# Kernel optimization log

Hardware: AMD Instinct MI355X
Metric: run time of the kernel (lower is better)

The kernel has to match this reference:

```python
import jax, jax.numpy as jnp
import numpy as np
from jax import lax


def setup_inputs() -> dict:
    key = jax.random.key(0)
    k1, k2 = jax.random.split(key)
    B, C, H, W = 4, 128, 128, 256
    features_1 = jax.random.normal(k1, (B, C, H, W), dtype=jnp.float32)
    features_2 = jax.random.normal(k2, (B, C, H, W), dtype=jnp.float32)
    return {"features_1": features_1, "features_2": features_2, "lvls": 64}


def reference(features_1, features_2, lvls):
    # Cost volume: cost[b, i, h, w] = mean_c f1[b,c,h,w] * f2[b,c,h,w-i] for w >= i, else 0.
    B, C, H, W = features_1.shape
    # Left-pad f2 along width with (lvls-1) zeros so shifted slices are static-size.
    f2_pad = jnp.pad(features_2, ((0, 0), (0, 0), (0, 0), (lvls - 1, 0)))

    def body(carry, i):
        # slice starting at (lvls-1-i) gives f2 shifted right by disparity i, zeros where w < i
        f2_shift = lax.dynamic_slice_in_dim(f2_pad, lvls - 1 - i, W, axis=3)
        cost_i = jnp.mean(features_1 * f2_shift, axis=1)  # [B, H, W]
        return carry, cost_i

    _, cost = lax.scan(body, None, jnp.arange(lvls))  # [lvls, B, H, W]
    return jnp.moveaxis(cost, 0, 1)  # [B, lvls, H, W]
```

## Files before the change

### kernel.cpp

```cpp
#include <hip/hip_runtime.h>
#include <hip/hip_bf16.h>


#define BDIM 4
#define CDIM 128
#define HDIM 128
#define WDIM 256
#define LVLS 64
#define HW   (HDIM * WDIM)
#define CHW  (CDIM * HDIM * WDIM)

typedef short  bf16x8 __attribute__((ext_vector_type(8)));
typedef float  f32x16 __attribute__((ext_vector_type(16)));

__device__ __forceinline__ short f2bf(float f) {
    __hip_bfloat16 h = __float2bfloat16(f);
    return __builtin_bit_cast(short, h);
}

__global__ __launch_bounds__(512, 4) void cost_volume_kernel(
    const float* __restrict__ f1, const float* __restrict__ f2,
    float* __restrict__ out)
{
    __shared__ float cost_lds[LVLS * WDIM];

    const int tid  = threadIdx.x;
    const int lane = tid & 63;
    const int wv   = tid >> 6;
    const int wg   = blockIdx.x;
    const int b    = wg >> 7;
    const int h    = wg & (HDIM - 1);

    const float* __restrict__ f1bh = f1 + (size_t)b * CHW + (size_t)h * WDIM;
    const float* __restrict__ f2bh = f2 + (size_t)b * CHW + (size_t)h * WDIM;

    const int wl    = lane & 31;
    const int wglob = wv * 32 + wl;
    const int koff  = (lane >> 5) * 8;

    const int tp0c = (wv - 2 < 0) ? 0 : wv - 2;
    const int tp1c = (wv - 1 < 0) ? 0 : wv - 1;
    const int tp2c = wv;

    const float* pB  = f1bh + (size_t)koff * HW + wglob;
    const float* pA0 = f2bh + (size_t)koff * HW + tp0c * 32 + wl;
    const float* pA1 = f2bh + (size_t)koff * HW + tp1c * 32 + wl;
    const float* pA2 = f2bh + (size_t)koff * HW + tp2c * 32 + wl;

    f32x16 acc0 = (f32x16)0.0f, acc1 = (f32x16)0.0f, acc2 = (f32x16)0.0f;

    #pragma unroll
    for (int kk = 0; kk < 8; ++kk) {
        const size_t kb = (size_t)(kk * 16) * HW;

        float rb[8], ra0[8], ra1[8], ra2[8];
        #pragma unroll
        for (int j = 0; j < 8; ++j) rb[j]  = pB [kb + (size_t)j * HW];
        #pragma unroll
        for (int j = 0; j < 8; ++j) ra0[j] = pA0[kb + (size_t)j * HW];
        #pragma unroll
        for (int j = 0; j < 8; ++j) ra1[j] = pA1[kb + (size_t)j * HW];
        #pragma unroll
        for (int j = 0; j < 8; ++j) ra2[j] = pA2[kb + (size_t)j * HW];

        bf16x8 fb, fa0, fa1, fa2;
        #pragma unroll
        for (int j = 0; j < 8; ++j) {
            fb[j]  = f2bf(rb[j]);
            fa0[j] = f2bf(ra0[j]);
            fa1[j] = f2bf(ra1[j]);
            fa2[j] = f2bf(ra2[j]);
        }

        acc0 = __builtin_amdgcn_mfma_f32_32x32x16_bf16(fa0, fb, acc0, 0, 0, 0);
        acc1 = __builtin_amdgcn_mfma_f32_32x32x16_bf16(fa1, fb, acc1, 0, 0, 0);
        acc2 = __builtin_amdgcn_mfma_f32_32x32x16_bf16(fa2, fb, acc2, 0, 0, 0);
    }


    if (wv < 2 && lane < 32) {
        #pragma unroll 1
        for (int i = 1; i < LVLS; ++i)
            if (i > wglob) cost_lds[i * WDIM + wglob] = 0.0f;
    }

    const int rbase = 4 * (lane >> 5);
    {
        const f32x16* accs[3] = { &acc0, &acc1, &acc2 };
        #pragma unroll
        for (int t = 0; t < 3; ++t) {
            const int tp = wv - 2 + t;
            if (tp >= 0) {
                const f32x16 a = *accs[t];
                #pragma unroll
                for (int r = 0; r < 16; ++r) {
                    const int prow = tp * 32 + (r & 3) + 8 * (r >> 2) + rbase;
                    const int i = wglob - prow;
                    if (i >= 0 && i < LVLS)
                        cost_lds[i * WDIM + wglob] = a[r] * (1.0f / CDIM);
                }
            }
        }
    }

    __syncthreads();

    const size_t obase = ((size_t)b * LVLS) * HW + (size_t)h * WDIM;
    #pragma unroll
    for (int rep = 0; rep < 8; ++rep) {
        const int idx = rep * 512 + tid;
        const int row = idx >> 6;
        const int w4  = idx & 63;
        const float4 v = *reinterpret_cast<const float4*>(&cost_lds[row * WDIM + w4 * 4]);
        *reinterpret_cast<float4*>(out + obase + (size_t)row * HW + w4 * 4) = v;
    }
}

extern "C" void kernel_launch(void* const* d_in, const int* in_sizes, int n_in,
                              void* d_out, int out_size, void* d_ws, size_t ws_size,
                              hipStream_t stream) {
    const float* f1 = (const float*)d_in[0];
    const float* f2 = (const float*)d_in[1];
    float* out = (float*)d_out;
    cost_volume_kernel<<<dim3(BDIM * HDIM), dim3(512), 0, stream>>>(f1, f2, out);
}
```

Measured before the change: 31.94 us.

## Stage feature tiles into LDS via async global_load_lds with double buffering

Each 16-channel slice of f1 and f2 is now loaded cooperatively into double-buffered LDS using global_load_lds. The next slice is prefetched while MFMAs run on the current one. This replaces direct per-lane global loads, which fetched each f2 column up to three times, so every byte is read from global memory once and load latency overlaps compute. In exchange there is a __syncthreads per iteration, extra LDS reads with possible bank conflicts, and reuse of the same LDS buffer for the cost output.

```diff
diff --git a/kernel.cpp b/kernel.cpp
--- a/kernel.cpp
+++ b/kernel.cpp
@@ -13,6 +13,9 @@
 typedef short  bf16x8 __attribute__((ext_vector_type(8)));
 typedef float  f32x16 __attribute__((ext_vector_type(16)));
 
+typedef __attribute__((address_space(1))) const unsigned int guint;
+typedef __attribute__((address_space(3))) unsigned int luint;
+
 __device__ __forceinline__ short f2bf(float f) {
     __hip_bfloat16 h = __float2bfloat16(f);
     return __builtin_bit_cast(short, h);
@@ -22,7 +25,7 @@
     const float* __restrict__ f1, const float* __restrict__ f2,
     float* __restrict__ out)
 {
-    __shared__ float cost_lds[LVLS * WDIM];
+    __shared__ float lds[16384];
 
     const int tid  = threadIdx.x;
     const int lane = tid & 63;
@@ -40,43 +43,57 @@
 
     const int tp0c = (wv - 2 < 0) ? 0 : wv - 2;
     const int tp1c = (wv - 1 < 0) ? 0 : wv - 1;
-    const int tp2c = wv;
-
-    const float* pB  = f1bh + (size_t)koff * HW + wglob;
-    const float* pA0 = f2bh + (size_t)koff * HW + tp0c * 32 + wl;
-    const float* pA1 = f2bh + (size_t)koff * HW + tp1c * 32 + wl;
-    const float* pA2 = f2bh + (size_t)koff * HW + tp2c * 32 + wl;
+    const int c0 = tp0c * 32 + wl;
+    const int c1 = tp1c * 32 + wl;
+    const int c2 = wv * 32 + wl;
 
     f32x16 acc0 = (f32x16)0.0f, acc1 = (f32x16)0.0f, acc2 = (f32x16)0.0f;
 
+    const int r0 = wv * 2;
+    #define STAGE(bb, kk)                                                        \
+        do {                                                                     \
+            _Pragma("unroll")                                                    \
+            for (int rr = 0; rr < 2; ++rr) {                                     \
+                const int r = r0 + rr;                                           \
+                const float* g1 = f1bh + (size_t)((kk) * 16 + r) * HW + lane * 4;\
+                const float* g2 = f2bh + (size_t)((kk) * 16 + r) * HW + lane * 4;\
+                float* l1 = &lds[(bb) * 8192 + r * 256];                         \
+                float* l2 = &lds[(bb) * 8192 + 4096 + r * 256];                  \
+                __builtin_amdgcn_global_load_lds((guint*)g1, (luint*)l1, 16, 0, 0);\
+                __builtin_amdgcn_global_load_lds((guint*)g2, (luint*)l2, 16, 0, 0);\
+            }                                                                    \
+        } while (0)
+
+    STAGE(0, 0);
+    __syncthreads();
+
     #pragma unroll
     for (int kk = 0; kk < 8; ++kk) {
-        const size_t kb = (size_t)(kk * 16) * HW;
+        const int bb = kk & 1;
+        if (kk < 7) STAGE(bb ^ 1, kk + 1);
 
-        float rb[8], ra0[8], ra1[8], ra2[8];
-        #pragma unroll
-        for (int j = 0; j < 8; ++j) rb[j]  = pB [kb + (size_t)j * HW];
-        #pragma unroll
-        for (int j = 0; j < 8; ++j) ra0[j] = pA0[kb + (size_t)j * HW];
-        #pragma unroll
-        for (int j = 0; j < 8; ++j) ra1[j] = pA1[kb + (size_t)j * HW];
-        #pragma unroll
-        for (int j = 0; j < 8; ++j) ra2[j] = pA2[kb + (size_t)j * HW];
+        const float* L1 = &lds[bb * 8192];
+        const float* L2 = &lds[bb * 8192 + 4096];
 
         bf16x8 fb, fa0, fa1, fa2;
         #pragma unroll
         for (int j = 0; j < 8; ++j) {
-            fb[j]  = f2bf(rb[j]);
-            fa0[j] = f2bf(ra0[j]);
-            fa1[j] = f2bf(ra1[j]);
-            fa2[j] = f2bf(ra2[j]);
+            const int k = koff + j;
+            fb[j]  = f2bf(L1[k * 256 + wglob]);
+            fa0[j] = f2bf(L2[k * 256 + c0]);
+            fa1[j] = f2bf(L2[k * 256 + c1]);
+            fa2[j] = f2bf(L2[k * 256 + c2]);
         }
 
         acc0 = __builtin_amdgcn_mfma_f32_32x32x16_bf16(fa0, fb, acc0, 0, 0, 0);
         acc1 = __builtin_amdgcn_mfma_f32_32x32x16_bf16(fa1, fb, acc1, 0, 0, 0);
         acc2 = __builtin_amdgcn_mfma_f32_32x32x16_bf16(fa2, fb, acc2, 0, 0, 0);
+
+        __syncthreads();
     }
 
+
+    float* cost_lds = lds;
 
     if (wv < 2 && lane < 32) {
         #pragma unroll 1
```

Measured after the change: 32.40 us. No clear change (+1.4%).

## Stage bf16-packed channel slices through double-buffered LDS with prefetched vector loads

Applied to the files above, without the earlier changes.

Replaces per-lane scalar global loads, where each f2 element was loaded up to three times by different waves, with cooperative float4 global loads. Each wave loads two channel rows, packs them to bf16 pairs and writes them into a double-buffered LDS stage; MFMA operands are then read from LDS. Loads are issued up to three stages ahead, with barriers between stages. Output stores become nontemporal. This adds per-stage block barriers and LDS traffic in exchange for coalesced, deduplicated global reads.

```diff
diff --git a/kernel.cpp b/kernel.cpp
--- a/kernel.cpp
+++ b/kernel.cpp
@@ -10,19 +10,24 @@
 #define HW   (HDIM * WDIM)
 #define CHW  (CDIM * HDIM * WDIM)
 
-typedef short  bf16x8 __attribute__((ext_vector_type(8)));
-typedef float  f32x16 __attribute__((ext_vector_type(16)));
+typedef short    bf16x8 __attribute__((ext_vector_type(8)));
+typedef float    f32x16 __attribute__((ext_vector_type(16)));
+typedef float    f32x4  __attribute__((ext_vector_type(4)));
+typedef unsigned u32x4  __attribute__((ext_vector_type(4)));
 
-__device__ __forceinline__ short f2bf(float f) {
-    __hip_bfloat16 h = __float2bfloat16(f);
-    return __builtin_bit_cast(short, h);
+__device__ __forceinline__ unsigned packbf(float lo, float hi) {
+    unsigned a = (unsigned)(unsigned short)__builtin_bit_cast(unsigned short, __float2bfloat16(lo));
+    unsigned b = (unsigned)(unsigned short)__builtin_bit_cast(unsigned short, __float2bfloat16(hi));
+    return a | (b << 16);
 }
 
 __global__ __launch_bounds__(512, 4) void cost_volume_kernel(
     const float* __restrict__ f1, const float* __restrict__ f2,
     float* __restrict__ out)
 {
-    __shared__ float cost_lds[LVLS * WDIM];
+    __shared__ __align__(16) char lds_raw[65536];
+    unsigned* stage = (unsigned*)lds_raw;
+    float*    cost  = (float*)lds_raw;
 
     const int tid  = threadIdx.x;
     const int lane = tid & 63;
@@ -36,52 +41,84 @@
 
     const int wl    = lane & 31;
     const int wglob = wv * 32 + wl;
-    const int koff  = (lane >> 5) * 8;
+    const int krow  = (lane >> 5) * 4;
 
-    const int tp0c = (wv - 2 < 0) ? 0 : wv - 2;
-    const int tp1c = (wv - 1 < 0) ? 0 : wv - 1;
-    const int tp2c = wv;
-
-    const float* pB  = f1bh + (size_t)koff * HW + wglob;
-    const float* pA0 = f2bh + (size_t)koff * HW + tp0c * 32 + wl;
-    const float* pA1 = f2bh + (size_t)koff * HW + tp1c * 32 + wl;
-    const float* pA2 = f2bh + (size_t)koff * HW + tp2c * 32 + wl;
+    const int c0 = ((wv - 2 < 0) ? 0 : wv - 2) * 32 + wl;
+    const int c1 = ((wv - 1 < 0) ? 0 : wv - 1) * 32 + wl;
+    const int c2 = wv * 32 + wl;
 
     f32x16 acc0 = (f32x16)0.0f, acc1 = (f32x16)0.0f, acc2 = (f32x16)0.0f;
 
+    f32x4 L1a[2], L1b[2], L2a[2], L2b[2];
+
+    #define ISSUE(s) do {                                                          \
+        const float* g1 = f1bh + (size_t)((s) * 16 + 2 * wv) * HW + lane * 4;      \
+        const float* g2 = f2bh + (size_t)((s) * 16 + 2 * wv) * HW + lane * 4;      \
+        L1a[(s) & 1] = *(const f32x4*)g1; L1b[(s) & 1] = *(const f32x4*)(g1 + HW); \
+        L2a[(s) & 1] = *(const f32x4*)g2; L2b[(s) & 1] = *(const f32x4*)(g2 + HW); \
+    } while (0)
+
+    #define WRITE(s) do {                                                          \
+        const int bb_ = (s) & 1;                                                   \
+        unsigned* p1 = stage + bb_ * 4096 + wv * 256 + (lane << 2);                \
+        u32x4 w1 = { packbf(L1a[bb_].x, L1b[bb_].x), packbf(L1a[bb_].y, L1b[bb_].y),\
+                     packbf(L1a[bb_].z, L1b[bb_].z), packbf(L1a[bb_].w, L1b[bb_].w) };\
+        *(u32x4*)p1 = w1;                                                          \
+        u32x4 w2 = { packbf(L2a[bb_].x, L2b[bb_].x), packbf(L2a[bb_].y, L2b[bb_].y),\
+                     packbf(L2a[bb_].z, L2b[bb_].z), packbf(L2a[bb_].w, L2b[bb_].w) };\
+        *(u32x4*)(p1 + 2048) = w2;                                                 \
+    } while (0)
+
+    ISSUE(0); ISSUE(1);
+    WRITE(0);
+    ISSUE(2);
+    asm volatile("s_waitcnt lgkmcnt(0)" ::: "memory");
+    __builtin_amdgcn_sched_barrier(0);
+    __builtin_amdgcn_s_barrier();
+    __builtin_amdgcn_sched_barrier(0);
+
     #pragma unroll
     for (int kk = 0; kk < 8; ++kk) {
-        const size_t kb = (size_t)(kk * 16) * HW;
+        if (kk < 7) WRITE(kk + 1);
+        if (kk + 3 <= 7) ISSUE(kk + 3);
 
-        float rb[8], ra0[8], ra1[8], ra2[8];
+        const int bb = kk & 1;
+        const unsigned* sb = stage + bb * 4096;
+        u32x4 wb, wa0, wa1, wa2;
         #pragma unroll
-        for (int j = 0; j < 8; ++j) rb[j]  = pB [kb + (size_t)j * HW];
-        #pragma unroll
-        for (int j = 0; j < 8; ++j) ra0[j] = pA0[kb + (size_t)j * HW];
-        #pragma unroll
-        for (int j = 0; j < 8; ++j) ra1[j] = pA1[kb + (size_t)j * HW];
-        #pragma unroll
-        for (int j = 0; j < 8; ++j) ra2[j] = pA2[kb + (size_t)j * HW];
+        for (int d = 0; d < 4; ++d) {
+            wb[d]  = sb[(krow + d) * 256 + wglob];
+            wa0[d] = sb[2048 + (krow + d) * 256 + c0];
+            wa1[d] = sb[2048 + (krow + d) * 256 + c1];
+            wa2[d] = sb[2048 + (krow + d) * 256 + c2];
+        }
+        asm volatile("s_waitcnt lgkmcnt(0)" ::: "memory");
+        __builtin_amdgcn_sched_barrier(0);
 
-        bf16x8 fb, fa0, fa1, fa2;
-        #pragma unroll
-        for (int j = 0; j < 8; ++j) {
-            fb[j]  = f2bf(rb[j]);
-            fa0[j] = f2bf(ra0[j]);
-            fa1[j] = f2bf(ra1[j]);
-            fa2[j] = f2bf(ra2[j]);
-        }
-
+        const bf16x8 fb  = __builtin_bit_cast(bf16x8, wb);
+        const bf16x8 fa0 = __builtin_bit_cast(bf16x8, wa0);
+        const bf16x8 fa1 = __builtin_bit_cast(bf16x8, wa1);
+        const bf16x8 fa2 = __builtin_bit_cast(bf16x8, wa2);
         acc0 = __builtin_amdgcn_mfma_f32_32x32x16_bf16(fa0, fb, acc0, 0, 0, 0);
         acc1 = __builtin_amdgcn_mfma_f32_32x32x16_bf16(fa1, fb, acc1, 0, 0, 0);
         acc2 = __builtin_amdgcn_mfma_f32_32x32x16_bf16(fa2, fb, acc2, 0, 0, 0);
+
+        if (kk < 7) {
+            __builtin_amdgcn_sched_barrier(0);
+            __builtin_amdgcn_s_barrier();
+            __builtin_amdgcn_sched_barrier(0);
+        }
     }
 
+    #undef ISSUE
+    #undef WRITE
+
+    __syncthreads();
 
     if (wv < 2 && lane < 32) {
         #pragma unroll 1
         for (int i = 1; i < LVLS; ++i)
-            if (i > wglob) cost_lds[i * WDIM + wglob] = 0.0f;
+            if (i > wglob) cost[i * WDIM + wglob] = 0.0f;
     }
 
     const int rbase = 4 * (lane >> 5);
@@ -97,7 +134,7 @@
                     const int prow = tp * 32 + (r & 3) + 8 * (r >> 2) + rbase;
                     const int i = wglob - prow;
                     if (i >= 0 && i < LVLS)
-                        cost_lds[i * WDIM + wglob] = a[r] * (1.0f / CDIM);
+                        cost[i * WDIM + wglob] = a[r] * (1.0f / CDIM);
                 }
             }
         }
@@ -111,8 +148,8 @@
         const int idx = rep * 512 + tid;
         const int row = idx >> 6;
         const int w4  = idx & 63;
-        const float4 v = *reinterpret_cast<const float4*>(&cost_lds[row * WDIM + w4 * 4]);
-        *reinterpret_cast<float4*>(out + obase + (size_t)row * HW + w4 * 4) = v;
+        const f32x4 v = *reinterpret_cast<const f32x4*>(&cost[row * WDIM + w4 * 4]);
+        __builtin_nontemporal_store(v, reinterpret_cast<f32x4*>(out + obase + (size_t)row * HW + w4 * 4));
     }
 }
 
```

Result: no change. 31.46 us (-1.5%).

## Split each row into single-wave blocks with per-strip LDS and nontemporal stores

Applied to the files above, without the earlier changes.

Each 512-thread workgroup per (b,h) row becomes eight independent 64-thread blocks, one per 32-column strip. Each block keeps a 64x32 LDS strip, so the workgroup barrier becomes a wave-local LDS fence. Block indices are remapped so that consecutive blocks land on different rows. Output writes now use nontemporal stores. The aim is to remove barrier stalls and the large per-block LDS footprint, and to improve occupancy and scheduling. In exchange there are eight times as many tiny blocks with more launch granularity, and the f2 data shared between neighbouring strips is no longer reused within a block.

```diff
diff --git a/kernel.cpp b/kernel.cpp
--- a/kernel.cpp
+++ b/kernel.cpp
@@ -9,45 +9,54 @@
 #define LVLS 64
 #define HW   (HDIM * WDIM)
 #define CHW  (CDIM * HDIM * WDIM)
+#define NWORK (BDIM * HDIM * 8)
 
-typedef short  bf16x8 __attribute__((ext_vector_type(8)));
-typedef float  f32x16 __attribute__((ext_vector_type(16)));
+typedef short    bf16x8 __attribute__((ext_vector_type(8)));
+typedef float    f32x16 __attribute__((ext_vector_type(16)));
+typedef float    f32x4  __attribute__((ext_vector_type(4)));
 
 __device__ __forceinline__ short f2bf(float f) {
     __hip_bfloat16 h = __float2bfloat16(f);
     return __builtin_bit_cast(short, h);
 }
 
-__global__ __launch_bounds__(512, 4) void cost_volume_kernel(
+__device__ __forceinline__ void lds_fence() {
+    asm volatile("s_waitcnt lgkmcnt(0)" ::: "memory");
+    __builtin_amdgcn_sched_barrier(0);
+}
+
+__global__ __launch_bounds__(64, 4) void cost_volume_kernel(
     const float* __restrict__ f1, const float* __restrict__ f2,
     float* __restrict__ out)
 {
-    __shared__ float cost_lds[LVLS * WDIM];
+    __shared__ float strip[LVLS * 32];
 
-    const int tid  = threadIdx.x;
-    const int lane = tid & 63;
-    const int wv   = tid >> 6;
-    const int wg   = blockIdx.x;
-    const int b    = wg >> 7;
-    const int h    = wg & (HDIM - 1);
+    const int lane = threadIdx.x;
+
+    const int bid  = blockIdx.x;
+    const int work = (bid & 7) * (NWORK / 8) + (bid >> 3);
+
+    const int wt = work & 7;
+    const int h  = (work >> 3) & (HDIM - 1);
+    const int b  = work >> 10;
 
     const float* __restrict__ f1bh = f1 + (size_t)b * CHW + (size_t)h * WDIM;
     const float* __restrict__ f2bh = f2 + (size_t)b * CHW + (size_t)h * WDIM;
 
     const int wl    = lane & 31;
-    const int wglob = wv * 32 + wl;
+    const int wglob = wt * 32 + wl;
     const int koff  = (lane >> 5) * 8;
 
-    const int tp0c = (wv - 2 < 0) ? 0 : wv - 2;
-    const int tp1c = (wv - 1 < 0) ? 0 : wv - 1;
-    const int tp2c = wv;
+    const int c0 = ((wt - 2 < 0) ? 0 : wt - 2) * 32 + wl;
+    const int c1 = ((wt - 1 < 0) ? 0 : wt - 1) * 32 + wl;
+    const int c2 = wt * 32 + wl;
+
+    f32x16 acc0 = (f32x16)0.0f, acc1 = (f32x16)0.0f, acc2 = (f32x16)0.0f;
 
     const float* pB  = f1bh + (size_t)koff * HW + wglob;
-    const float* pA0 = f2bh + (size_t)koff * HW + tp0c * 32 + wl;
-    const float* pA1 = f2bh + (size_t)koff * HW + tp1c * 32 + wl;
-    const float* pA2 = f2bh + (size_t)koff * HW + tp2c * 32 + wl;
-
-    f32x16 acc0 = (f32x16)0.0f, acc1 = (f32x16)0.0f, acc2 = (f32x16)0.0f;
+    const float* pA0 = f2bh + (size_t)koff * HW + c0;
+    const float* pA1 = f2bh + (size_t)koff * HW + c1;
+    const float* pA2 = f2bh + (size_t)koff * HW + c2;
 
     #pragma unroll
     for (int kk = 0; kk < 8; ++kk) {
@@ -78,18 +87,18 @@
     }
 
 
-    if (wv < 2 && lane < 32) {
-        #pragma unroll 1
-        for (int i = 1; i < LVLS; ++i)
-            if (i > wglob) cost_lds[i * WDIM + wglob] = 0.0f;
-    }
+    #pragma unroll
+    for (int it = 0; it < 8; ++it)
+        reinterpret_cast<f32x4*>(strip)[it * 64 + lane] = (f32x4)0.0f;
+
+    lds_fence();
 
     const int rbase = 4 * (lane >> 5);
     {
         const f32x16* accs[3] = { &acc0, &acc1, &acc2 };
         #pragma unroll
         for (int t = 0; t < 3; ++t) {
-            const int tp = wv - 2 + t;
+            const int tp = wt - 2 + t;
             if (tp >= 0) {
                 const f32x16 a = *accs[t];
                 #pragma unroll
@@ -97,22 +106,22 @@
                     const int prow = tp * 32 + (r & 3) + 8 * (r >> 2) + rbase;
                     const int i = wglob - prow;
                     if (i >= 0 && i < LVLS)
-                        cost_lds[i * WDIM + wglob] = a[r] * (1.0f / CDIM);
+                        strip[i * 32 + wl] = a[r] * (1.0f / CDIM);
                 }
             }
         }
     }
 
-    __syncthreads();
+    lds_fence();
 
-    const size_t obase = ((size_t)b * LVLS) * HW + (size_t)h * WDIM;
+    const size_t obase = (size_t)b * LVLS * HW + (size_t)h * WDIM + wt * 32;
     #pragma unroll
-    for (int rep = 0; rep < 8; ++rep) {
-        const int idx = rep * 512 + tid;
-        const int row = idx >> 6;
-        const int w4  = idx & 63;
-        const float4 v = *reinterpret_cast<const float4*>(&cost_lds[row * WDIM + w4 * 4]);
-        *reinterpret_cast<float4*>(out + obase + (size_t)row * HW + w4 * 4) = v;
+    for (int it = 0; it < 8; ++it) {
+        const int idx = it * 64 + lane;
+        const int row = idx >> 3;
+        const int w4  = idx & 7;
+        const f32x4 v = *reinterpret_cast<const f32x4*>(&strip[row * 32 + w4 * 4]);
+        __builtin_nontemporal_store(v, reinterpret_cast<f32x4*>(out + obase + (size_t)row * HW + w4 * 4));
     }
 }
 
@@ -122,5 +131,5 @@
     const float* f1 = (const float*)d_in[0];
     const float* f2 = (const float*)d_in[1];
     float* out = (float*)d_out;
-    cost_volume_kernel<<<dim3(BDIM * HDIM), dim3(512), 0, stream>>>(f1, f2, out);
+    cost_volume_kernel<<<dim3(NWORK), dim3(64), 0, stream>>>(f1, f2, out);
 }
```

Measured after the change: 30.46 us. 4.6% less time.
